# Kernel optimization log

Measured on AMD Instinct MI355X. Metric: run time of the kernel, lower is better.

The kernel has to match this reference:

```python
import jax, jax.numpy as jnp
import numpy as np

B, N, E = 128, 196, 2048   # batch, num_features (14x14), encoder_dim
D, A = 512, 512            # decoder_dim, attention_dim


def setup_inputs() -> dict:
    key = jax.random.key(0)
    ks = jax.random.split(key, 8)
    s_e = 1.0 / np.sqrt(E)
    s_d = 1.0 / np.sqrt(D)
    s_a = 1.0 / np.sqrt(A)
    return {
        "encoder_out": jax.random.normal(ks[0], (B, N, E), dtype=jnp.float32),
        "decoder_hidden": jax.random.normal(ks[1], (B, D), dtype=jnp.float32),
        "We": jax.random.uniform(ks[2], (E, A), jnp.float32, -s_e, s_e),
        "be": jax.random.uniform(ks[3], (A,), jnp.float32, -s_e, s_e),
        "Wd": jax.random.uniform(ks[4], (D, A), jnp.float32, -s_d, s_d),
        "bd": jax.random.uniform(ks[5], (A,), jnp.float32, -s_d, s_d),
        "Wf": jax.random.uniform(ks[6], (A, 1), jnp.float32, -s_a, s_a),
        "bf": jax.random.uniform(ks[7], (1,), jnp.float32, -s_a, s_a),
    }


def reference(encoder_out, decoder_hidden, We, be, Wd, bd, Wf, bf):
    # att1: [B,N,A] projection of encoder features
    att1 = jnp.einsum('bne,ea->bna', encoder_out, We) + be
    # att2: [B,A] projection of decoder state, broadcast over N
    att2 = decoder_hidden @ Wd + bd
    att = jnp.tanh(att1 + att2[:, None, :])          # [B,N,A]
    scores = jnp.einsum('bna,ao->bno', att, Wf) + bf  # [B,N,1]
    alpha = jax.nn.softmax(scores, axis=1)            # softmax over num_features
    context = jnp.sum(encoder_out * alpha, axis=1)    # [B,E]
    return (context, alpha)
```

## Files before the change

kernel.cpp:

```cpp
#include <hip/hip_runtime.h>
#include <hip/hip_bf16.h>
#include <stdint.h>

#define B_   128
#define N_   196
#define E_   2048
#define D_   512
#define A_   512
#define MTOT (B_ * N_)

typedef short  short8  __attribute__((ext_vector_type(8)));
typedef float  floatx4 __attribute__((ext_vector_type(4)));

__device__ __forceinline__ unsigned short f2bf(float f) {
    union { float f; uint32_t u; } v; v.f = f;
    uint32_t r = v.u + 0x7FFFu + ((v.u >> 16) & 1u);
    return (unsigned short)(r >> 16);
}

__device__ __forceinline__ uint32_t pkbf(float a, float b) {
    uint32_t ua = __float_as_uint(a) + 0x8000u;
    uint32_t ub = __float_as_uint(b) + 0x8000u;
    return __builtin_amdgcn_perm(ub, ua, 0x07060302u);
}

__global__ void transcvt_k(const float* __restrict__ We, unsigned short* __restrict__ WeT2) {
    const int t   = threadIdx.x;
    const int l15 = t & 15;
    const int q4  = (t >> 4) & 3;
    const int g   = t >> 6;
    const int tile = blockIdx.x;
    const int kk   = blockIdx.y * 4 + g;
    const int a  = tile * 16 + l15;
    const int e0 = kk * 32 + q4 * 8;
    union { unsigned short us[8]; short8 s; } pk;
#pragma unroll
    for (int j = 0; j < 8; ++j)
        pk.us[j] = f2bf(We[(size_t)(e0 + j) * A_ + a]);
    *(short8*)(WeT2 + (size_t)tile * 32768 + kk * 512 + q4 * 128 + l15 * 8) = pk.s;
}

__launch_bounds__(512)
__global__ void att2_k(const float* __restrict__ dh, const float* __restrict__ Wd,
                       const float* __restrict__ bd, const float* __restrict__ be,
                       float* __restrict__ att2p) {
    const int b = blockIdx.x, t = threadIdx.x;
    __shared__ float sdh[D_];
    sdh[t] = dh[b * D_ + t];
    __syncthreads();
    float acc = 0.f;
#pragma unroll 8
    for (int d = 0; d < D_; ++d) acc += sdh[d] * Wd[(size_t)d * A_ + t];
    att2p[(size_t)b * A_ + t] = acc + bd[t] + be[t];
}

__launch_bounds__(256, 3)
__global__ void score_gemm(const float* __restrict__ enc,
                           const unsigned short* __restrict__ WeT2,
                           const float* __restrict__ att2p,
                           const float* __restrict__ Wf,
                           float* __restrict__ scoresP) {
    __shared__ __align__(16) char sMem[8192 + 16384];
    __shared__ float sPart[4][64];

    const int t   = threadIdx.x;
    const int w   = t >> 6;
    const int l   = t & 63;
    const int l15 = l & 15;
    const int q4  = l >> 4;
    const int row0 = blockIdx.y * 64;
    const int col0 = blockIdx.x * 256;

    floatx4 acc[4][4] = {};

    const float* aSrc[2];
    int aDst[2];
#pragma unroll
    for (int h = 0; h < 2; ++h) {
        aSrc[h] = enc + (size_t)(row0 + w * 16 + l15) * E_ + (4 * h + q4) * 4;
        aDst[h] = w * 2048 + h * 1024 + l * 16;
    }
    const unsigned short* bSrc[4];
    int bDst[4];
#pragma unroll
    for (int j = 0; j < 4; ++j) {
        bSrc[j] = WeT2 + (size_t)((col0 >> 4) + w * 4 + j) * 32768 + l * 8;
        bDst[j] = 8192 + (w * 4 + j) * 1024 + l * 16;
    }

    const int offAlo = (2 * q4) * 256 + l15 * 16;
    const int offB   = 8192 + w * 4096 + q4 * 256 + l15 * 16;

    for (int kk = 0; kk < 64; ++kk) {
#pragma unroll
        for (int h = 0; h < 2; ++h)
            __builtin_amdgcn_global_load_lds(
                (const __attribute__((address_space(1))) uint32_t*)(aSrc[h] + kk * 32),
                (__attribute__((address_space(3))) uint32_t*)(sMem + aDst[h]), 16, 0, 0);
#pragma unroll
        for (int j = 0; j < 4; ++j)
            __builtin_amdgcn_global_load_lds(
                (const __attribute__((address_space(1))) uint32_t*)(bSrc[j] + kk * 512),
                (__attribute__((address_space(3))) uint32_t*)(sMem + bDst[j]), 16, 0, 0);
        __syncthreads();

        short8 bfr[4];
        union { uint32_t u[4]; short8 s; } af[4];
#pragma unroll
        for (int ni = 0; ni < 4; ++ni)
            bfr[ni] = *(const short8*)(sMem + offB + ni * 1024);
#pragma unroll
        for (int mi = 0; mi < 4; ++mi) {
            float4 lo = *(const float4*)(sMem + mi * 2048 + offAlo);
            float4 hi = *(const float4*)(sMem + mi * 2048 + offAlo + 256);
            af[mi].u[0] = pkbf(lo.x, lo.y);
            af[mi].u[1] = pkbf(lo.z, lo.w);
            af[mi].u[2] = pkbf(hi.x, hi.y);
            af[mi].u[3] = pkbf(hi.z, hi.w);
        }
#pragma unroll
        for (int mi = 0; mi < 4; ++mi) {
            acc[mi][0] = __builtin_amdgcn_mfma_f32_16x16x32_bf16(af[mi].s, bfr[0], acc[mi][0], 0, 0, 0);
            acc[mi][1] = __builtin_amdgcn_mfma_f32_16x16x32_bf16(af[mi].s, bfr[1], acc[mi][1], 0, 0, 0);
            acc[mi][2] = __builtin_amdgcn_mfma_f32_16x16x32_bf16(af[mi].s, bfr[2], acc[mi][2], 0, 0, 0);
            acc[mi][3] = __builtin_amdgcn_mfma_f32_16x16x32_bf16(af[mi].s, bfr[3], acc[mi][3], 0, 0, 0);
        }
        __syncthreads();
    }

    const int cbase = col0 + w * 64;
    float wfv[4];
#pragma unroll
    for (int ni = 0; ni < 4; ++ni) wfv[ni] = Wf[cbase + ni * 16 + l15];

#pragma unroll
    for (int mi = 0; mi < 4; ++mi) {
#pragma unroll
        for (int r = 0; r < 4; ++r) {
            const int m    = mi * 16 + q4 * 4 + r;
            const int grow = row0 + m;
            const int bb   = grow / N_;
            const float* a2 = att2p + (size_t)bb * A_ + cbase;
            float s = 0.f;
#pragma unroll
            for (int ni = 0; ni < 4; ++ni) {
                float v  = acc[mi][ni][r] + a2[ni * 16 + l15];
                float e  = __expf(2.f * v);
                float th = 1.f - 2.f / (e + 1.f);
                s += th * wfv[ni];
            }
            s += __shfl_xor(s, 1);
            s += __shfl_xor(s, 2);
            s += __shfl_xor(s, 4);
            s += __shfl_xor(s, 8);
            if (l15 == 0) sPart[w][m] = s;
        }
    }
    __syncthreads();
    if (t < 64) {
        float v = sPart[0][t] + sPart[1][t] + sPart[2][t] + sPart[3][t];
        scoresP[(size_t)blockIdx.x * MTOT + row0 + t] = v;
    }
}

__global__ void softmax_k(const float* __restrict__ sp, float* __restrict__ alpha) {
    const int b = blockIdx.x, t = threadIdx.x;
    const int w = t >> 6, l = t & 63;
    __shared__ float red[8];
    float v = -3.0e38f;
    if (t < N_) v = sp[b * N_ + t] + sp[MTOT + b * N_ + t];
    float m = v;
#pragma unroll
    for (int off = 32; off >= 1; off >>= 1) m = fmaxf(m, __shfl_xor(m, off));
    if (l == 0) red[w] = m;
    __syncthreads();
    m = fmaxf(fmaxf(red[0], red[1]), fmaxf(red[2], red[3]));
    float e = 0.f;
    if (t < N_) e = __expf(v - m);
    float s = e;
#pragma unroll
    for (int off = 32; off >= 1; off >>= 1) s += __shfl_xor(s, off);
    if (l == 0) red[4 + w] = s;
    __syncthreads();
    s = red[4] + red[5] + red[6] + red[7];
    if (t < N_) alpha[b * N_ + t] = e / s;
}

__launch_bounds__(256)
__global__ void context_k(const float* __restrict__ enc, const float* __restrict__ alpha,
                          float* __restrict__ ctx) {
    const int chunk = blockIdx.x, b = blockIdx.y;
    const int t = threadIdx.x, tn = t >> 6, tc = t & 63;
    __shared__ float  sAl[N_];
    __shared__ float4 sRed[256];
    if (t < N_) sAl[t] = alpha[b * N_ + t];
    __syncthreads();
    const float* base = enc + (size_t)b * N_ * E_ + chunk * 256 + tc * 4;
    float4 a = make_float4(0.f, 0.f, 0.f, 0.f);
#pragma unroll 7
    for (int n = tn; n < N_; n += 4) {
        float  al = sAl[n];
        float4 v  = *(const float4*)(base + (size_t)n * E_);
        a.x += al * v.x; a.y += al * v.y; a.z += al * v.z; a.w += al * v.w;
    }
    sRed[t] = a;
    __syncthreads();
    if (t < 64) {
        float4 r0 = sRed[t], r1 = sRed[t + 64], r2 = sRed[t + 128], r3 = sRed[t + 192];
        float4 o = make_float4(r0.x + r1.x + r2.x + r3.x, r0.y + r1.y + r2.y + r3.y,
                               r0.z + r1.z + r2.z + r3.z, r0.w + r1.w + r2.w + r3.w);
        *(float4*)(ctx + (size_t)b * E_ + chunk * 256 + t * 4) = o;
    }
}

extern "C" void kernel_launch(void* const* d_in, const int* in_sizes, int n_in,
                              void* d_out, int out_size, void* d_ws, size_t ws_size,
                              hipStream_t stream) {
    const float* enc = (const float*)d_in[0];
    const float* dh  = (const float*)d_in[1];
    const float* We  = (const float*)d_in[2];
    const float* be  = (const float*)d_in[3];
    const float* Wd  = (const float*)d_in[4];
    const float* bd  = (const float*)d_in[5];
    const float* Wf  = (const float*)d_in[6];

    float* out   = (float*)d_out;
    float* ctx   = out;
    float* alpha = out + B_ * E_;

    char* ws = (char*)d_ws;
    unsigned short* WeT2 = (unsigned short*)ws;
    float* att2p         = (float*)(ws + (2u << 20));
    float* scoresP       = (float*)(ws + (2u << 20) + (256u << 10));

    transcvt_k <<<dim3(32, 16),       256, 0, stream>>>(We, WeT2);
    att2_k     <<<dim3(B_),           512, 0, stream>>>(dh, Wd, bd, be, att2p);
    score_gemm <<<dim3(2, MTOT / 64), 256, 0, stream>>>(enc, WeT2, att2p, Wf, scoresP);
    softmax_k  <<<dim3(B_),           256, 0, stream>>>(scoresP, alpha);
    context_k  <<<dim3(E_ / 256, B_), 256, 0, stream>>>(enc, alpha, ctx);
}
```

Measured before the change: 466.2 us.

## Double-buffer A tile in LDS and register-prefetch B fragments directly from global

The score GEMM main loop now double-buffers the encoder (A) tile in LDS, so the next k-slice load is issued before the current one is consumed, with one barrier per iteration. The pre-transposed bf16 weight (B) fragments are no longer staged through LDS: each wave loads them straight from global into registers, one iteration ahead. This hides global latency behind the MFMA work and cuts LDS size and traffic. In exchange it uses more registers for the prefetched B fragments and relies on global loads arriving in time without LDS reuse.

```diff
diff --git a/kernel.cpp b/kernel.cpp
--- a/kernel.cpp
+++ b/kernel.cpp
@@ -60,7 +60,7 @@
                            const float* __restrict__ att2p,
                            const float* __restrict__ Wf,
                            float* __restrict__ scoresP) {
-    __shared__ __align__(16) char sMem[8192 + 16384];
+    __shared__ __align__(16) char sMem[2][8192];
     __shared__ float sPart[4][64];
 
     const int t   = threadIdx.x;
@@ -80,51 +80,59 @@
         aSrc[h] = enc + (size_t)(row0 + w * 16 + l15) * E_ + (4 * h + q4) * 4;
         aDst[h] = w * 2048 + h * 1024 + l * 16;
     }
-    const unsigned short* bSrc[4];
-    int bDst[4];
-#pragma unroll
-    for (int j = 0; j < 4; ++j) {
-        bSrc[j] = WeT2 + (size_t)((col0 >> 4) + w * 4 + j) * 32768 + l * 8;
-        bDst[j] = 8192 + (w * 4 + j) * 1024 + l * 16;
-    }
+
+    const int ctBase = (col0 >> 4) + w * 4;
+    const unsigned short* pbB[4];
+#pragma unroll
+    for (int ni = 0; ni < 4; ++ni)
+        pbB[ni] = WeT2 + (size_t)(ctBase + ni) * 32768 + l * 8;
 
     const int offAlo = (2 * q4) * 256 + l15 * 16;
-    const int offB   = 8192 + w * 4096 + q4 * 256 + l15 * 16;
+
+#pragma unroll
+    for (int h = 0; h < 2; ++h)
+        __builtin_amdgcn_global_load_lds(
+            (const __attribute__((address_space(1))) uint32_t*)(aSrc[h]),
+            (__attribute__((address_space(3))) uint32_t*)(&sMem[0][0] + aDst[h]), 16, 0, 0);
+    short8 Bcur[4], Bnxt[4];
+#pragma unroll
+    for (int ni = 0; ni < 4; ++ni) Bcur[ni] = *(const short8*)(pbB[ni]);
+    __syncthreads();
 
     for (int kk = 0; kk < 64; ++kk) {
-#pragma unroll
-        for (int h = 0; h < 2; ++h)
-            __builtin_amdgcn_global_load_lds(
-                (const __attribute__((address_space(1))) uint32_t*)(aSrc[h] + kk * 32),
-                (__attribute__((address_space(3))) uint32_t*)(sMem + aDst[h]), 16, 0, 0);
-#pragma unroll
-        for (int j = 0; j < 4; ++j)
-            __builtin_amdgcn_global_load_lds(
-                (const __attribute__((address_space(1))) uint32_t*)(bSrc[j] + kk * 512),
-                (__attribute__((address_space(3))) uint32_t*)(sMem + bDst[j]), 16, 0, 0);
-        __syncthreads();
-
-        short8 bfr[4];
+        if (kk < 63) {
+#pragma unroll
+            for (int h = 0; h < 2; ++h)
+                __builtin_amdgcn_global_load_lds(
+                    (const __attribute__((address_space(1))) uint32_t*)(aSrc[h] + (kk + 1) * 32),
+                    (__attribute__((address_space(3))) uint32_t*)(&sMem[(kk + 1) & 1][0] + aDst[h]),
+                    16, 0, 0);
+        }
+        const char* aBuf = &sMem[kk & 1][0];
         union { uint32_t u[4]; short8 s; } af[4];
 #pragma unroll
-        for (int ni = 0; ni < 4; ++ni)
-            bfr[ni] = *(const short8*)(sMem + offB + ni * 1024);
-#pragma unroll
         for (int mi = 0; mi < 4; ++mi) {
-            float4 lo = *(const float4*)(sMem + mi * 2048 + offAlo);
-            float4 hi = *(const float4*)(sMem + mi * 2048 + offAlo + 256);
+            float4 lo = *(const float4*)(aBuf + mi * 2048 + offAlo);
+            float4 hi = *(const float4*)(aBuf + mi * 2048 + offAlo + 256);
             af[mi].u[0] = pkbf(lo.x, lo.y);
             af[mi].u[1] = pkbf(lo.z, lo.w);
             af[mi].u[2] = pkbf(hi.x, hi.y);
             af[mi].u[3] = pkbf(hi.z, hi.w);
         }
+        if (kk < 63) {
+#pragma unroll
+            for (int ni = 0; ni < 4; ++ni)
+                Bnxt[ni] = *(const short8*)(pbB[ni] + (kk + 1) * 512);
+        }
 #pragma unroll
         for (int mi = 0; mi < 4; ++mi) {
-            acc[mi][0] = __builtin_amdgcn_mfma_f32_16x16x32_bf16(af[mi].s, bfr[0], acc[mi][0], 0, 0, 0);
-            acc[mi][1] = __builtin_amdgcn_mfma_f32_16x16x32_bf16(af[mi].s, bfr[1], acc[mi][1], 0, 0, 0);
-            acc[mi][2] = __builtin_amdgcn_mfma_f32_16x16x32_bf16(af[mi].s, bfr[2], acc[mi][2], 0, 0, 0);
-            acc[mi][3] = __builtin_amdgcn_mfma_f32_16x16x32_bf16(af[mi].s, bfr[3], acc[mi][3], 0, 0, 0);
-        }
+            acc[mi][0] = __builtin_amdgcn_mfma_f32_16x16x32_bf16(af[mi].s, Bcur[0], acc[mi][0], 0, 0, 0);
+            acc[mi][1] = __builtin_amdgcn_mfma_f32_16x16x32_bf16(af[mi].s, Bcur[1], acc[mi][1], 0, 0, 0);
+            acc[mi][2] = __builtin_amdgcn_mfma_f32_16x16x32_bf16(af[mi].s, Bcur[2], acc[mi][2], 0, 0, 0);
+            acc[mi][3] = __builtin_amdgcn_mfma_f32_16x16x32_bf16(af[mi].s, Bcur[3], acc[mi][3], 0, 0, 0);
+        }
+#pragma unroll
+        for (int ni = 0; ni < 4; ++ni) Bcur[ni] = Bnxt[ni];
         __syncthreads();
     }
 
```

New measurement: 484.4 us. 1.04x slower.
